# Optimization experiments

Hardware: AMD Instinct MI355X
Metric: run time of the kernel (lower is better)

Reference implementation:

```python
import jax, jax.numpy as jnp
import numpy as np

B, K, D, LS, NL = 32, 64, 256, 128, 2


def _xavier(key, shape):
    # torch xavier_uniform for Linear weight [out, in]
    fan_out, fan_in = shape[-2], shape[-1]
    lim = float(np.sqrt(6.0 / (fan_in + fan_out)))
    return jax.random.uniform(key, shape, jnp.float32, -lim, lim)


def setup_inputs():
    key = jax.random.key(0)
    ks = jax.random.split(key, 32)
    inp = {
        "X": jax.random.normal(ks[0], (B, K, D), jnp.float32),
        # per-layer stacked params [NL, ...]
        "k_w": _xavier(ks[1], (NL, D, D)),
        "q_w": _xavier(ks[2], (NL, D, D)),
        "rv_w1": _xavier(ks[3], (NL, D, 2 * D)),
        "rv_b1": jnp.zeros((NL, D), jnp.float32),
        "rv_w2": _xavier(ks[4], (NL, D, D)),
        "rv_b2": jnp.zeros((NL, D), jnp.float32),
        "ln_g": jnp.ones((NL, D), jnp.float32),
        "ln_b": jnp.zeros((NL, D), jnp.float32),
        "mlp_w1": _xavier(ks[5], (NL, D, D)),
        "mlp_b1": jnp.zeros((NL, D), jnp.float32),
        "mlp_w2": _xavier(ks[6], (NL, D, D)),
        "mlp_b2": jnp.zeros((NL, D), jnp.float32),
        "proj_w": _xavier(ks[7], (LS, D)),
        "proj_b": jnp.zeros((LS,), jnp.float32),
        "mu_w": _xavier(ks[8], (LS, LS)),
        "mu_b": jnp.zeros((LS,), jnp.float32),
        "sp_w": _xavier(ks[9], (LS, LS)),
        "sp_b": jnp.zeros((LS,), jnp.float32),
    }
    return inp


def _gelu(x):
    return jax.nn.gelu(x, approximate=False)


def _layernorm(x, g, b, eps=1e-5):
    m = jnp.mean(x, axis=-1, keepdims=True)
    v = jnp.mean((x - m) ** 2, axis=-1, keepdims=True)
    return (x - m) / jnp.sqrt(v + eps) * g + b


def _block(x, kw, qw, rw1, rb1, rw2, rb2, lg, lb, mw1, mb1, mw2, mb2):
    scale = D ** (-0.5)
    x_orig = x
    # pairwise difference r[b,i,j,:] = x[b,i]-x[b,j]
    r = x[:, :, None, :] - x[:, None, :, :]                      # [B,K,K,D]
    xi = jnp.broadcast_to(x[:, :, None, :], (B, K, K, D))
    cat = jnp.concatenate([xi, r], axis=-1)                      # [B,K,K,2D]
    v = _gelu(jnp.einsum('bijc,dc->bijd', cat, rw1) + rb1)
    v = jnp.einsum('bijd,ed->bije', v, rw2) + rb2                # [B,K,K,D]
    k = jnp.einsum('bid,ed->bie', x, kw)
    q = jnp.einsum('bid,ed->bie', x, qw) * scale
    attn = jax.nn.softmax(jnp.einsum('bid,bjd->bij', q, k), axis=2)
    agg = jnp.einsum('bij,bijd->bid', attn, v)
    h = _layernorm(x_orig + agg, lg, lb)
    h = jnp.einsum('bid,ed->bie', _gelu(jnp.einsum('bid,ed->bie', h, mw1) + mb1), mw2) + mb2
    return x_orig + h


def reference(X, k_w, q_w, rv_w1, rv_b1, rv_w2, rv_b2, ln_g, ln_b,
              mlp_w1, mlp_b1, mlp_w2, mlp_b2, proj_w, proj_b,
              mu_w, mu_b, sp_w, sp_b):
    x = X
    for i in range(NL):
        x = _block(x, k_w[i], q_w[i], rv_w1[i], rv_b1[i], rv_w2[i], rv_b2[i],
                   ln_g[i], ln_b[i], mlp_w1[i], mlp_b1[i], mlp_w2[i], mlp_b2[i])
    s = jnp.sum(x, axis=1)                                        # [B,D]
    h = _gelu(s @ proj_w.T + proj_b)                              # [B,LS]
    mu = h @ mu_w.T + mu_b
    scale = jax.nn.softplus(h @ sp_w.T + sp_b)
    return (mu, scale)
```

## Files before the change

kernel.cpp:

```cpp
#include <hip/hip_runtime.h>
#include <hip/hip_bf16.h>

#define NL 2

using bf16 = __hip_bfloat16;
typedef short bf16x8 __attribute__((ext_vector_type(8)));
typedef float f32x4 __attribute__((ext_vector_type(4)));

__device__ __forceinline__ float bfu(unsigned short u) { return __uint_as_float(((unsigned)u) << 16); }

__device__ __forceinline__ unsigned short bfr(float v) {
  unsigned u = __float_as_uint(v);
  u += 0x7FFFu + ((u >> 16) & 1u);
  return (unsigned short)(u >> 16);
}

__device__ __forceinline__ float gelu_s(float x) {
  float e = __expf(-1.702f * x);
  return x * __builtin_amdgcn_rcpf(1.0f + e);
}

__device__ __forceinline__ float gelu_e(float x) {
  return 0.5f * x * (1.0f + erff(x * 0.7071067811865475f));
}

__device__ __forceinline__ float load_f(const void* p, int i, int fl) {
  if (fl) return bfu(((const unsigned short*)p)[i]);
  return ((const float*)p)[i];
}

__device__ __forceinline__ int block_detect(const void* X) {
  __shared__ int bad_s;
  if (threadIdx.x == 0) bad_s = 0;
  __syncthreads();
  if (threadIdx.x < 256) {
    const float v = bfu(((const unsigned short*)X)[threadIdx.x]);
    if (!(fabsf(v) < 1e6f)) atomicOr(&bad_s, 1);
  }
  __syncthreads();
  return bad_s ? 0 : 1;
}

__device__ __forceinline__ void stage_split4(unsigned short (&aF)[2][4096], int row, int d0, float4 v) {
  ushort4 h, lo;
  h.x = bfr(v.x); h.y = bfr(v.y); h.z = bfr(v.z); h.w = bfr(v.w);
  lo.x = bfr(v.x - bfu(h.x)); lo.y = bfr(v.y - bfu(h.y));
  lo.z = bfr(v.z - bfu(h.z)); lo.w = bfr(v.w - bfu(h.w));
  const int kt = d0 >> 5, lane = row | (((d0 >> 3) & 3) << 4), j = d0 & 7;
  *(ushort4*)&aF[0][kt*512 + lane*8 + j] = h;
  *(ushort4*)&aF[1][kt*512 + lane*8 + j] = lo;
}

__global__ __launch_bounds__(256) void prep_kernel(
    const void* __restrict__ X, const void* __restrict__ kw, const void* __restrict__ qw,
    const void* __restrict__ rw1, const void* __restrict__ rw2, const void* __restrict__ mw1,
    const void* __restrict__ mw2, const void* __restrict__ pw, const void* __restrict__ muw,
    const void* __restrict__ spw,
    const void* __restrict__ rb1, const void* __restrict__ rb2, const void* __restrict__ lng,
    const void* __restrict__ lnb, const void* __restrict__ mb1, const void* __restrict__ mb2,
    const void* __restrict__ pb, const void* __restrict__ mub, const void* __restrict__ spb,
    unsigned short* __restrict__ wfb, unsigned short* __restrict__ w3b,
    float* __restrict__ wh, float* __restrict__ bc)
{
  __shared__ __align__(16) char psm[65536];
  const int fl = block_detect(X);
  const int t = threadIdx.x;
  int blk = blockIdx.x;

  if (blk < 16) {
    unsigned short* ls = (unsigned short*)psm;
    unsigned* lsu = (unsigned*)psm;
    const int l = blk >> 3, kt = blk & 7;
    if (fl) {
      #pragma unroll
      for (int s = 0; s < 4; ++s) {
        const unsigned* sp = (const unsigned*)((s == 0) ? kw : (s == 1) ? qw : rw1);
        const int rstr = (s < 2) ? 128 : 256;
        const int coff = ((s == 3) ? 128 : 0) + kt*16;
        for (int i = t; i < 4096; i += 256) {
          const int e = i >> 4, d2 = i & 15;
          lsu[s*4096 + i] = sp[(l*256 + e)*rstr + coff + d2];
        }
      }
    } else {
      #pragma unroll
      for (int s = 0; s < 4; ++s) {
        const float* sp = (const float*)((s == 0) ? kw : (s == 1) ? qw : rw1);
        const int rstr = (s < 2) ? 256 : 512;
        const int coff = ((s == 3) ? 256 : 0) + kt*32;
        for (int i = t; i < 4096; i += 256) {
          const int e = i >> 4, d2 = i & 15;
          const float f0 = sp[(l*256 + e)*rstr + coff + d2*2];
          const float f1 = sp[(l*256 + e)*rstr + coff + d2*2 + 1];
          lsu[s*4096 + i] = (unsigned)bfr(f0) | ((unsigned)bfr(f1) << 16);
        }
      }
    }
    __syncthreads();
    unsigned* outp = (unsigned*)wfb + (l*8 + kt)*16384;
    for (int f2 = t; f2 < 16384; f2 += 256) {
      const int j2 = f2 & 3, lane = (f2 >> 2) & 63, ntg = f2 >> 8;
      const int seg = ntg >> 4;
      const int e = (ntg & 15)*16 + (lane & 15);
      const int dl = ((lane >> 4) & 3)*8 + j2*2;
      unsigned short r0 = ls[seg*8192 + e*32 + dl];
      unsigned short r1 = ls[seg*8192 + e*32 + dl + 1];
      if (seg == 1) { r0 = bfr(bfu(r0)*0.0625f); r1 = bfr(bfu(r1)*0.0625f); }
      else if (seg == 2) {
        const unsigned short w0 = ls[3*8192 + e*32 + dl];
        const unsigned short w1 = ls[3*8192 + e*32 + dl + 1];
        r0 = bfr(bfu(r0) + bfu(w0)); r1 = bfr(bfu(r1) + bfu(w1));
      }
      outp[f2] = (unsigned)r0 | ((unsigned)r1 << 16);
    }
    return;
  }
  blk -= 16;
  if (blk < 48) {
    unsigned short* ls = (unsigned short*)psm;
    unsigned* lsu = (unsigned*)psm;
    const int l3 = blk >> 3, kt = blk & 7;
    const int l = l3 / 3, gm = l3 % 3;
    const void* src = (gm == 0) ? rw2 : (gm == 1) ? mw1 : mw2;
    if (fl) {
      const unsigned* sp = (const unsigned*)src;
      for (int i = t; i < 4096; i += 256) {
        const int e = i >> 4, d2 = i & 15;
        lsu[i] = sp[(l*256 + e)*128 + kt*16 + d2];
      }
    } else {
      const float* sp = (const float*)src;
      for (int i = t; i < 4096; i += 256) {
        const int e = i >> 4, d2 = i & 15;
        const float f0 = sp[(l*256 + e)*256 + kt*32 + d2*2];
        const float f1 = sp[(l*256 + e)*256 + kt*32 + d2*2 + 1];
        lsu[i] = (unsigned)bfr(f0) | ((unsigned)bfr(f1) << 16);
      }
    }
    __syncthreads();
    unsigned* outp = (unsigned*)w3b + (l3*8 + kt)*4096;
    for (int f2 = t; f2 < 4096; f2 += 256) {
      const int j2 = f2 & 3, lane = (f2 >> 2) & 63, nt = f2 >> 8;
      const int e = nt*16 + (lane & 15);
      const int dl = ((lane >> 4) & 3)*8 + j2*2;
      outp[f2] = (unsigned)ls[e*32 + dl] | ((unsigned)ls[e*32 + dl + 1] << 16);
    }
    return;
  }
  blk -= 48;
  if (blk < 24) {
    float* lsf = (float*)psm;
    if (blk < 8) {
      const int l0 = blk*16;
      if (fl) {
        const unsigned* sp = (const unsigned*)pw;
        for (int i = t; i < 2048; i += 256) {
          const int ll = i >> 7, d2 = i & 127;
          const unsigned u = sp[(l0 + ll)*128 + d2];
          lsf[ll*256 + d2*2]     = __uint_as_float(u << 16);
          lsf[ll*256 + d2*2 + 1] = __uint_as_float(u & 0xffff0000u);
        }
      } else {
        const float* sp = (const float*)pw;
        for (int i = t; i < 4096; i += 256) {
          const int ll = i >> 8, d = i & 255;
          lsf[ll*256 + d] = sp[(l0 + ll)*256 + d];
        }
      }
      __syncthreads();
      for (int i = t; i < 4096; i += 256) {
        const int d = i >> 4, ll = i & 15;
        wh[d*128 + l0 + ll] = lsf[ll*256 + d];
      }
    } else {
      const int grp = blk - 8;
      const int isSp = grp >> 3;
      const int l0 = (grp & 7)*16;
      const void* src = isSp ? spw : muw;
      const int off = isSp ? 49152 : 32768;
      if (fl) {
        const unsigned* sp = (const unsigned*)src;
        for (int i = t; i < 1024; i += 256) {
          const int ll = i >> 6, c2 = i & 63;
          const unsigned u = sp[(l0 + ll)*64 + c2];
          lsf[ll*128 + c2*2]     = __uint_as_float(u << 16);
          lsf[ll*128 + c2*2 + 1] = __uint_as_float(u & 0xffff0000u);
        }
      } else {
        const float* sp = (const float*)src;
        for (int i = t; i < 2048; i += 256) {
          const int ll = i >> 7, c = i & 127;
          lsf[ll*128 + c] = sp[(l0 + ll)*128 + c];
        }
      }
      __syncthreads();
      for (int i = t; i < 2048; i += 256) {
        const int c = i >> 4, ll = i & 15;
        wh[off + c*128 + l0 + ll] = lsf[ll*128 + c];
      }
    }
    return;
  }
  for (int i = t; i < 3456; i += 256) {
    const void* src; int off;
    if (i < 512)       { src = rb1; off = i; }
    else if (i < 1024) { src = rb2; off = i - 512; }
    else if (i < 1536) { src = lng; off = i - 1024; }
    else if (i < 2048) { src = lnb; off = i - 1536; }
    else if (i < 2560) { src = mb1; off = i - 2048; }
    else if (i < 3072) { src = mb2; off = i - 2560; }
    else if (i < 3200) { src = pb;  off = i - 3072; }
    else if (i < 3328) { src = mub; off = i - 3200; }
    else               { src = spb; off = i - 3328; }
    bc[i] = load_f(src, off, fl);
  }
}

template<bool SPLIT>
__device__ __forceinline__ void k1_body(
    const unsigned short (&aF)[2][4096],
    const unsigned short* __restrict__ wfb, const float* __restrict__ bc,
    float* __restrict__ kq, float* __restrict__ Pf, unsigned* __restrict__ Qpk,
    int l, int row0, int t)
{
  const int w = t >> 6, l64 = t & 63;
  const int col = l64 & 15, quad = l64 >> 4;
  f32x4 acc[8];
  #pragma unroll
  for (int i = 0; i < 8; ++i) acc[i] = (f32x4){0.f, 0.f, 0.f, 0.f};
  for (int kt = 0; kt < 8; ++kt) {
    const bf16x8 ah = *(const bf16x8*)&aF[0][kt*512 + l64*8];
    bf16x8 al;
    if (SPLIT) al = *(const bf16x8*)&aF[1][kt*512 + l64*8];
    #pragma unroll
    for (int i = 0; i < 8; ++i) {
      const int ntg = w*8 + i;
      const bf16x8 b = *(const bf16x8*)&wfb[((l*8 + kt)*64 + ntg)*512 + l64*8];
      acc[i] = __builtin_amdgcn_mfma_f32_16x16x32_bf16(ah, b, acc[i], 0, 0, 0);
      if (SPLIT) acc[i] = __builtin_amdgcn_mfma_f32_16x16x32_bf16(al, b, acc[i], 0, 0, 0);
    }
  }
  #pragma unroll
  for (int i = 0; i < 8; ++i) {
    const int ntg = w*8 + i;
    if (ntg < 32) {
      const int n = ntg*16 + col;
      #pragma unroll
      for (int r = 0; r < 4; ++r)
        kq[(size_t)(row0 + quad*4 + r)*512 + n] = acc[i][r];
    } else if (ntg < 48) {
      const int c = (ntg - 32)*16 + col;
      const float bias = bc[l*256 + c];
      #pragma unroll
      for (int r = 0; r < 4; ++r)
        Pf[(size_t)(row0 + quad*4 + r)*256 + c] = acc[i][r] + bias;
    } else {
      #pragma unroll
      for (int r = 0; r < 4; ++r) {
        const float v = acc[i][r];
        const float pv = __shfl_xor(v, 1, 64);
        if (!(col & 1)) {
          const unsigned uu = (unsigned)bfr(v) | ((unsigned)bfr(pv) << 16);
          Qpk[(size_t)(row0 + quad*4 + r)*128 + (ntg - 48)*8 + (col >> 1)] = uu;
        }
      }
    }
  }
}

__global__ __launch_bounds__(512) void k1l0(
    const void* __restrict__ X, const unsigned short* __restrict__ wfb,
    const float* __restrict__ bc, float* __restrict__ kq, float* __restrict__ Pf,
    unsigned* __restrict__ Qpk)
{
  const int fl = block_detect(X);
  __shared__ __align__(16) unsigned short aF[2][4096];
  const int t = threadIdx.x;
  const int row0 = blockIdx.x * 16;
  if (fl) {
    const int c = t;
    const int row = c >> 5, d0 = (c & 31) * 8;
    const uint4 u = *(const uint4*)((const unsigned*)X + (size_t)(row0 + row)*128 + (c & 31)*4);
    const int kt = d0 >> 5, lane = row | (((d0 >> 3) & 3) << 4);
    *(uint4*)&aF[0][kt*512 + lane*8] = u;
  } else {
    for (int i = t; i < 1024; i += 512) {
      const int row = i >> 6, d0 = (i & 63) * 4;
      const float4 v = *(const float4*)((const float*)X + (size_t)(row0 + row)*256 + d0);
      stage_split4(aF, row, d0, v);
    }
  }
  __syncthreads();
  if (fl) k1_body<false>(aF, wfb, bc, kq, Pf, Qpk, 0, row0, t);
  else    k1_body<true >(aF, wfb, bc, kq, Pf, Qpk, 0, row0, t);
}

__global__ __launch_bounds__(256) void k23_attn(
    const float* __restrict__ kq, const float* __restrict__ Pf,
    const unsigned* __restrict__ Qpk, float* __restrict__ g)
{
  __shared__ unsigned qls[8192];
  __shared__ float qs[4][256];
  __shared__ float sc[4][64];
  __shared__ float als[4][64];
  const int t = threadIdx.x;
  const int b = (int)blockIdx.x >> 4, rq = (int)blockIdx.x & 15;
  const int base = b << 6, i0 = rq * 4;
  {
    const float4* src = (const float4*)(Qpk + (size_t)base*128);
    float4* dst = (float4*)qls;
    for (int i = t; i < 2048; i += 256) dst[i] = src[i];
  }
  for (int i = t; i < 1024; i += 256)
    qs[i >> 8][i & 255] = kq[(size_t)(base + i0 + (i >> 8))*512 + 256 + (i & 255)];
  __syncthreads();

  {
    const int w = t >> 6, lane = t & 63;
    const int jl = lane & 15, part = lane >> 4;
    const int j = w*16 + jl;
    const float* krow = kq + (size_t)(base + j)*512 + part*64;
    float s0 = 0.f, s1 = 0.f, s2 = 0.f, s3 = 0.f;
    for (int dd = 0; dd < 64; dd += 4) {
      const float4 kv = *(const float4*)&krow[dd];
      const float4 q0 = *(const float4*)&qs[0][part*64 + dd];
      const float4 q1 = *(const float4*)&qs[1][part*64 + dd];
      const float4 q2 = *(const float4*)&qs[2][part*64 + dd];
      const float4 q3 = *(const float4*)&qs[3][part*64 + dd];
      s0 = fmaf(kv.x, q0.x, s0); s0 = fmaf(kv.y, q0.y, s0); s0 = fmaf(kv.z, q0.z, s0); s0 = fmaf(kv.w, q0.w, s0);
      s1 = fmaf(kv.x, q1.x, s1); s1 = fmaf(kv.y, q1.y, s1); s1 = fmaf(kv.z, q1.z, s1); s1 = fmaf(kv.w, q1.w, s1);
      s2 = fmaf(kv.x, q2.x, s2); s2 = fmaf(kv.y, q2.y, s2); s2 = fmaf(kv.z, q2.z, s2); s2 = fmaf(kv.w, q2.w, s2);
      s3 = fmaf(kv.x, q3.x, s3); s3 = fmaf(kv.y, q3.y, s3); s3 = fmaf(kv.z, q3.z, s3); s3 = fmaf(kv.w, q3.w, s3);
    }
    s0 += __shfl_xor(s0, 16, 64); s0 += __shfl_xor(s0, 32, 64);
    s1 += __shfl_xor(s1, 16, 64); s1 += __shfl_xor(s1, 32, 64);
    s2 += __shfl_xor(s2, 16, 64); s2 += __shfl_xor(s2, 32, 64);
    s3 += __shfl_xor(s3, 16, 64); s3 += __shfl_xor(s3, 32, 64);
    if (part == 0) { sc[0][j] = s0; sc[1][j] = s1; sc[2][j] = s2; sc[3][j] = s3; }
  }
  __syncthreads();
  {
    const int row = t >> 6, j = t & 63;
    float s = sc[row][j];
    float m = s;
    #pragma unroll
    for (int off = 32; off; off >>= 1) m = fmaxf(m, __shfl_xor(m, off, 64));
    const float e = __expf(s - m);
    float ss = e;
    #pragma unroll
    for (int off = 32; off; off >>= 1) ss += __shfl_xor(ss, off, 64);
    als[row][j] = e / ss;
  }
  __syncthreads();

  const int rg = t >> 7, cp = t & 127;
  const int r0 = base + i0 + rg*2;
  const float2 P0 = *(const float2*)&Pf[(size_t)r0*256 + cp*2];
  const float2 P1 = *(const float2*)&Pf[(size_t)(r0 + 1)*256 + cp*2];
  const float A00 = -1.702f * P0.x, A01 = -1.702f * P0.y;
  const float A10 = -1.702f * P1.x, A11 = -1.702f * P1.y;
  const float* a0p = &als[rg*2][0];
  const float* a1p = &als[rg*2 + 1][0];
  float acc00 = 0.f, acc01 = 0.f, acc10 = 0.f, acc11 = 0.f;
  #pragma unroll 4
  for (int j = 0; j < 64; ++j) {
    const unsigned u = qls[j*128 + cp];
    const float w0 = a0p[j], w1 = a1p[j];
    const float q0 = __uint_as_float(u << 16);
    const float q1 = __uint_as_float(u & 0xffff0000u);
    const float s00 = __builtin_amdgcn_rcpf(1.f + __expf(fmaf(1.702f, q0, A00)));
    const float s01 = __builtin_amdgcn_rcpf(1.f + __expf(fmaf(1.702f, q1, A01)));
    const float s10 = __builtin_amdgcn_rcpf(1.f + __expf(fmaf(1.702f, q0, A10)));
    const float s11 = __builtin_amdgcn_rcpf(1.f + __expf(fmaf(1.702f, q1, A11)));
    acc00 = fmaf(w0 * (P0.x - q0), s00, acc00);
    acc01 = fmaf(w0 * (P0.y - q1), s01, acc01);
    acc10 = fmaf(w1 * (P1.x - q0), s10, acc10);
    acc11 = fmaf(w1 * (P1.y - q1), s11, acc11);
  }
  *(float2*)&g[(size_t)r0*256 + cp*2]       = make_float2(acc00, acc01);
  *(float2*)&g[(size_t)(r0 + 1)*256 + cp*2] = make_float2(acc10, acc11);
}

__device__ __forceinline__ void k4_gemm8(
    f32x4 acc[2], const unsigned short (&aF)[2][4096],
    const unsigned short* __restrict__ wg, int w, int l64)
{
  acc[0] = (f32x4){0.f, 0.f, 0.f, 0.f};
  acc[1] = (f32x4){0.f, 0.f, 0.f, 0.f};
  for (int kt = 0; kt < 8; ++kt) {
    const bf16x8 ah = *(const bf16x8*)&aF[0][kt*512 + l64*8];
    const bf16x8 al = *(const bf16x8*)&aF[1][kt*512 + l64*8];
    #pragma unroll
    for (int nt = 0; nt < 2; ++nt) {
      const bf16x8 b = *(const bf16x8*)&wg[((kt*16 + (w*2 + nt))*64 + l64)*8];
      acc[nt] = __builtin_amdgcn_mfma_f32_16x16x32_bf16(ah, b, acc[nt], 0, 0, 0);
      acc[nt] = __builtin_amdgcn_mfma_f32_16x16x32_bf16(al, b, acc[nt], 0, 0, 0);
    }
  }
}

template<bool ADAPT, bool TAIL>
__device__ __forceinline__ void k4_core(
    const float* __restrict__ g, const void* __restrict__ xin, int fl,
    float* __restrict__ xout, const unsigned short* __restrict__ wg,
    const float* __restrict__ bc, int l, int row0, int t,
    unsigned short (&aF)[2][4096], float* bufB, float (&mv)[16][2])
{
  const int w = t >> 6, l64 = t & 63;
  const int col = l64 & 15, quad = l64 >> 4;
  const float* rb2c = bc + 512  + l*256;
  const float* lngc = bc + 1024 + l*256;
  const float* lnbc = bc + 1536 + l*256;
  const float* mb1c = bc + 2048 + l*256;
  const float* mb2c = bc + 2560 + l*256;

  for (int i = t; i < 1024; i += 512) {
    const int row = i >> 6, d0 = (i & 63) * 4;
    stage_split4(aF, row, d0, *(const float4*)&g[(size_t)(row0 + row)*256 + d0]);
  }
  if (ADAPT && fl) {
    for (int c = t; c < 2048; c += 512) {
      const int row = c >> 7, dp = c & 127;
      const unsigned u = ((const unsigned*)xin)[(size_t)(row0 + row)*128 + dp];
      bufB[row*260 + dp*2]     = __uint_as_float(u << 16);
      bufB[row*260 + dp*2 + 1] = __uint_as_float(u & 0xffff0000u);
    }
  } else {
    for (int c = t; c < 1024; c += 512) {
      const int row = c >> 6, d0 = (c & 63) * 4;
      *(float4*)&bufB[row*260 + d0] = *(const float4*)((const float*)xin + (size_t)(row0 + row)*256 + d0);
    }
  }
  __syncthreads();
  float xtr[2][4];
  #pragma unroll
  for (int nt = 0; nt < 2; ++nt) {
    const int cn = (w*2 + nt)*16 + col;
    #pragma unroll
    for (int r = 0; r < 4; ++r) xtr[nt][r] = bufB[(quad*4 + r)*260 + cn];
  }
  __syncthreads();

  f32x4 acc[2];
  k4_gemm8(acc, aF, wg, w, l64);
  #pragma unroll
  for (int nt = 0; nt < 2; ++nt) {
    const int cn = (w*2 + nt)*16 + col;
    #pragma unroll
    for (int r = 0; r < 4; ++r)
      bufB[(quad*4 + r)*260 + cn] = acc[nt][r] + rb2c[cn] + xtr[nt][r];
  }
  __syncthreads();
  {
    const int row = t >> 5, part = t & 31;
    float s = 0.f, s2 = 0.f;
    #pragma unroll
    for (int kk = 0; kk < 8; ++kk) {
      const float v = bufB[row*260 + part + kk*32];
      s += v; s2 = fmaf(v, v, s2);
    }
    #pragma unroll
    for (int off = 16; off; off >>= 1) {
      s  += __shfl_xor(s, off, 32);
      s2 += __shfl_xor(s2, off, 32);
    }
    if (part == 0) {
      const float mu = s * (1.f/256.f);
      mv[row][0] = mu;
      mv[row][1] = rsqrtf(fmaf(-mu, mu, s2 * (1.f/256.f)) + 1e-5f);
    }
  }
  __syncthreads();
  for (int i = t; i < 1024; i += 512) {
    const int row = i >> 6, d0 = (i & 63) * 4;
    float4 v = *(const float4*)&bufB[row*260 + d0];
    const float m = mv[row][0], iv = mv[row][1];
    v.x = (v.x - m)*iv*lngc[d0]   + lnbc[d0];
    v.y = (v.y - m)*iv*lngc[d0+1] + lnbc[d0+1];
    v.z = (v.z - m)*iv*lngc[d0+2] + lnbc[d0+2];
    v.w = (v.w - m)*iv*lngc[d0+3] + lnbc[d0+3];
    stage_split4(aF, row, d0, v);
  }
  __syncthreads();
  k4_gemm8(acc, aF, wg + 65536, w, l64);
  #pragma unroll
  for (int nt = 0; nt < 2; ++nt) {
    const int cn = (w*2 + nt)*16 + col;
    #pragma unroll
    for (int r = 0; r < 4; ++r)
      bufB[(quad*4 + r)*260 + cn] = gelu_e(acc[nt][r] + mb1c[cn]);
  }
  __syncthreads();
  for (int i = t; i < 1024; i += 512) {
    const int row = i >> 6, d0 = (i & 63) * 4;
    stage_split4(aF, row, d0, *(const float4*)&bufB[row*260 + d0]);
  }
  __syncthreads();
  k4_gemm8(acc, aF, wg + 2*65536, w, l64);
  if (TAIL) {
    #pragma unroll
    for (int nt = 0; nt < 2; ++nt) {
      const int cn = (w*2 + nt)*16 + col;
      #pragma unroll
      for (int r = 0; r < 4; ++r)
        bufB[(quad*4 + r)*260 + cn] = acc[nt][r] + mb2c[cn] + xtr[nt][r];
    }
    __syncthreads();
    for (int i = t; i < 1024; i += 512) {
      const int row = i >> 6, d0 = (i & 63) * 4;
      const float4 v = *(const float4*)&bufB[row*260 + d0];
      *(float4*)&xout[(size_t)(row0 + row)*256 + d0] = v;
      stage_split4(aF, row, d0, v);
    }
    __syncthreads();
  } else {
    #pragma unroll
    for (int nt = 0; nt < 2; ++nt) {
      const int cn = (w*2 + nt)*16 + col;
      #pragma unroll
      for (int r = 0; r < 4; ++r)
        xout[(size_t)(row0 + quad*4 + r)*256 + cn] = acc[nt][r] + mb2c[cn] + xtr[nt][r];
    }
  }
}

__global__ __launch_bounds__(512) void k41_mix_kq(
    const float* __restrict__ g, const unsigned short* __restrict__ w3b,
    const unsigned short* __restrict__ wfb, const float* __restrict__ bc,
    const void* __restrict__ X, float* __restrict__ x,
    float* __restrict__ kq, float* __restrict__ Pf, unsigned* __restrict__ Qpk)
{
  const int fl = block_detect(X);
  __shared__ __align__(16) unsigned short aF[2][4096];
  __shared__ float bufB[16*260];
  __shared__ float mv[16][2];
  const int t = threadIdx.x;
  const int row0 = blockIdx.x * 16;
  k4_core<true, true>(g, X, fl, x, w3b, bc, 0, row0, t, aF, bufB, mv);
  k1_body<true>(aF, wfb, bc, kq, Pf, Qpk, 1, row0, t);
}

__global__ __launch_bounds__(512) void k4_fin(
    const float* __restrict__ g, const unsigned short* __restrict__ w3b,
    const float* __restrict__ bc, float* __restrict__ x)
{
  __shared__ __align__(16) unsigned short aF[2][4096];
  __shared__ float bufB[16*260];
  __shared__ float mv[16][2];
  const int t = threadIdx.x;
  const int row0 = blockIdx.x * 16;
  k4_core<false, false>(g, x, 0, x, w3b + 3*65536, bc, 1, row0, t, aF, bufB, mv);
}

__global__ __launch_bounds__(256) void k5_head(
    const float* __restrict__ x, const float* __restrict__ wh,
    const float* __restrict__ bc, const void* __restrict__ X,
    void* __restrict__ out)
{
  const int fl = block_detect(X);
  __shared__ float ss[256];
  __shared__ float hh[128];
  const int b = blockIdx.x, t = threadIdx.x;
  float s = 0.f;
  for (int i = 0; i < 64; ++i) s += x[(size_t)((b << 6) + i)*256 + t];
  ss[t] = s;
  __syncthreads();
  if (t < 128) {
    float acc = bc[3072 + t];
    const float* projT = wh;
    for (int d = 0; d < 256; ++d) acc = fmaf(ss[d], projT[d*128 + t], acc);
    hh[t] = gelu_e(acc);
  }
  __syncthreads();
  float v; int oidx;
  if (t < 128) {
    float acc = bc[3200 + t];
    const float* muT = wh + 32768;
    for (int c = 0; c < 128; ++c) acc = fmaf(hh[c], muT[c*128 + t], acc);
    v = acc; oidx = b*128 + t;
  } else {
    const int u = t - 128;
    float acc = bc[3328 + u];
    const float* spT = wh + 49152;
    for (int c = 0; c < 128; ++c) acc = fmaf(hh[c], spT[c*128 + u], acc);
    v = (acc > 20.f) ? acc : log1pf(__expf(acc));
    oidx = 4096 + b*128 + u;
  }
  if (fl) ((bf16*)out)[oidx] = __float2bfloat16(v);
  else    ((float*)out)[oidx] = v;
}

extern "C" void kernel_launch(void* const* d_in, const int* in_sizes, int n_in,
                              void* d_out, int out_size, void* d_ws, size_t ws_size,
                              hipStream_t stream)
{
  (void)in_sizes; (void)n_in; (void)out_size; (void)ws_size;
  float* ws    = (float*)d_ws;
  float* x     = ws + 16;
  float* kq    = x + 524288;
  float* Pf    = kq + 1048576;
  unsigned* Qpk = (unsigned*)(Pf + 524288);
  float* g     = (float*)(Qpk + 262144);
  unsigned short* wfb = (unsigned short*)(g + 524288);
  unsigned short* w3b = wfb + 524288;
  float* wh    = (float*)(w3b + 393216);
  float* bc    = wh + 65536;

  prep_kernel<<<dim3(89), dim3(256), 0, stream>>>(
      d_in[0], d_in[1], d_in[2], d_in[3], d_in[5], d_in[9], d_in[11],
      d_in[13], d_in[15], d_in[17],
      d_in[4], d_in[6], d_in[7], d_in[8], d_in[10], d_in[12],
      d_in[14], d_in[16], d_in[18],
      wfb, w3b, wh, bc);
  k1l0<<<dim3(128), dim3(512), 0, stream>>>(d_in[0], wfb, bc, kq, Pf, Qpk);
  k23_attn<<<dim3(512), dim3(256), 0, stream>>>(kq, Pf, Qpk, g);
  k41_mix_kq<<<dim3(128), dim3(512), 0, stream>>>(g, w3b, wfb, bc, d_in[0], x, kq, Pf, Qpk);
  k23_attn<<<dim3(512), dim3(256), 0, stream>>>(kq, Pf, Qpk, g);
  k4_fin<<<dim3(128), dim3(512), 0, stream>>>(g, w3b, bc, x);
  k5_head<<<dim3(32), dim3(256), 0, stream>>>(x, wh, bc, d_in[0], (void*)d_out);
}
```

Before: 213.8 us.

## Fuse all stages into one persistent kernel with global atomic barriers

Replaces the seven separate launches (prep, layer-0 kq, two attention passes, mix/kq, final mix, head) with a single 256-block persistent kernel. Stages are separated by a grid-wide barrier after weight prep and by per-batch-group atomic counters after that, so each group of 8 blocks advances on its own. Work is remapped to 512-thread blocks and the prep blocks' inner loops now stride by 512. This removes launch gaps and tail effects, but relies on all 256 blocks being co-resident and adds spin-wait cost plus an extra memset.

New measurement: 268.6 us. 1.26x slower.

```diff
diff --git a/kernel.cpp b/kernel.cpp
--- a/kernel.cpp
+++ b/kernel.cpp
@@ -1,7 +1,6 @@
 #include <hip/hip_runtime.h>
 #include <hip/hip_bf16.h>
 
-#define NL 2
 
 using bf16 = __hip_bfloat16;
 typedef short bf16x8 __attribute__((ext_vector_type(8)));
@@ -15,11 +14,6 @@
   return (unsigned short)(u >> 16);
 }
 
-__device__ __forceinline__ float gelu_s(float x) {
-  float e = __expf(-1.702f * x);
-  return x * __builtin_amdgcn_rcpf(1.0f + e);
-}
-
 __device__ __forceinline__ float gelu_e(float x) {
   return 0.5f * x * (1.0f + erff(x * 0.7071067811865475f));
 }
@@ -39,6 +33,18 @@
   }
   __syncthreads();
   return bad_s ? 0 : 1;
+}
+
+__device__ __forceinline__ void wsbar(unsigned* cnt, unsigned need) {
+  __syncthreads();
+  if (threadIdx.x == 0) {
+    __threadfence();
+    atomicAdd(cnt, 1u);
+    while (__hip_atomic_load(cnt, __ATOMIC_RELAXED, __HIP_MEMORY_SCOPE_AGENT) < need)
+      __builtin_amdgcn_s_sleep(2);
+    __threadfence();
+  }
+  __syncthreads();
 }
 
 __device__ __forceinline__ void stage_split4(unsigned short (&aF)[2][4096], int row, int d0, float4 v) {
@@ -51,86 +57,103 @@
   *(ushort4*)&aF[1][kt*512 + lane*8 + j] = lo;
 }
 
-__global__ __launch_bounds__(256) void prep_kernel(
-    const void* __restrict__ X, const void* __restrict__ kw, const void* __restrict__ qw,
-    const void* __restrict__ rw1, const void* __restrict__ rw2, const void* __restrict__ mw1,
-    const void* __restrict__ mw2, const void* __restrict__ pw, const void* __restrict__ muw,
-    const void* __restrict__ spw,
-    const void* __restrict__ rb1, const void* __restrict__ rb2, const void* __restrict__ lng,
-    const void* __restrict__ lnb, const void* __restrict__ mb1, const void* __restrict__ mb2,
-    const void* __restrict__ pb, const void* __restrict__ mub, const void* __restrict__ spb,
-    unsigned short* __restrict__ wfb, unsigned short* __restrict__ w3b,
-    float* __restrict__ wh, float* __restrict__ bc)
-{
-  __shared__ __align__(16) char psm[65536];
-  const int fl = block_detect(X);
-  const int t = threadIdx.x;
-  int blk = blockIdx.x;
-
+__device__ void prep_phase(
+    int blk, int t, int fl, char* psm,
+    const void* kw, const void* qw, const void* rw1, const void* rw2,
+    const void* mw1, const void* mw2, const void* pw, const void* muw, const void* spw,
+    const void* rb1, const void* rb2, const void* lng, const void* lnb,
+    const void* mb1, const void* mb2, const void* pb, const void* mub, const void* spb,
+    unsigned short* wfb, unsigned short* w3b, float* wh, float* bc)
+{
   if (blk < 16) {
     unsigned short* ls = (unsigned short*)psm;
     unsigned* lsu = (unsigned*)psm;
     const int l = blk >> 3, kt = blk & 7;
-    if (fl) {
-      #pragma unroll
-      for (int s = 0; s < 4; ++s) {
-        const unsigned* sp = (const unsigned*)((s == 0) ? kw : (s == 1) ? qw : rw1);
-        const int rstr = (s < 2) ? 128 : 256;
-        const int coff = ((s == 3) ? 128 : 0) + kt*16;
-        for (int i = t; i < 4096; i += 256) {
-          const int e = i >> 4, d2 = i & 15;
-          lsu[s*4096 + i] = sp[(l*256 + e)*rstr + coff + d2];
-        }
-      }
-    } else {
-      #pragma unroll
-      for (int s = 0; s < 4; ++s) {
-        const float* sp = (const float*)((s == 0) ? kw : (s == 1) ? qw : rw1);
-        const int rstr = (s < 2) ? 256 : 512;
-        const int coff = ((s == 3) ? 256 : 0) + kt*32;
-        for (int i = t; i < 4096; i += 256) {
-          const int e = i >> 4, d2 = i & 15;
-          const float f0 = sp[(l*256 + e)*rstr + coff + d2*2];
-          const float f1 = sp[(l*256 + e)*rstr + coff + d2*2 + 1];
-          lsu[s*4096 + i] = (unsigned)bfr(f0) | ((unsigned)bfr(f1) << 16);
-        }
-      }
-    }
-    __syncthreads();
-    unsigned* outp = (unsigned*)wfb + (l*8 + kt)*16384;
-    for (int f2 = t; f2 < 16384; f2 += 256) {
-      const int j2 = f2 & 3, lane = (f2 >> 2) & 63, ntg = f2 >> 8;
-      const int seg = ntg >> 4;
-      const int e = (ntg & 15)*16 + (lane & 15);
-      const int dl = ((lane >> 4) & 3)*8 + j2*2;
-      unsigned short r0 = ls[seg*8192 + e*32 + dl];
-      unsigned short r1 = ls[seg*8192 + e*32 + dl + 1];
-      if (seg == 1) { r0 = bfr(bfu(r0)*0.0625f); r1 = bfr(bfu(r1)*0.0625f); }
-      else if (seg == 2) {
-        const unsigned short w0 = ls[3*8192 + e*32 + dl];
-        const unsigned short w1 = ls[3*8192 + e*32 + dl + 1];
-        r0 = bfr(bfu(r0) + bfu(w0)); r1 = bfr(bfu(r1) + bfu(w1));
-      }
-      outp[f2] = (unsigned)r0 | ((unsigned)r1 << 16);
+    #pragma unroll
+    for (int pass = 0; pass < 2; ++pass) {
+      if (pass == 0) {
+        if (fl) {
+          #pragma unroll
+          for (int s = 0; s < 2; ++s) {
+            const unsigned* sp = (const unsigned*)((s == 0) ? kw : qw);
+            for (int i = t; i < 4096; i += 512) {
+              const int e = i >> 4, d2 = i & 15;
+              lsu[s*4096 + i] = sp[(l*256 + e)*128 + kt*16 + d2];
+            }
+          }
+        } else {
+          #pragma unroll
+          for (int s = 0; s < 2; ++s) {
+            const float* sp = (const float*)((s == 0) ? kw : qw);
+            for (int i = t; i < 4096; i += 512) {
+              const int e = i >> 4, d2 = i & 15;
+              const float f0 = sp[(l*256 + e)*256 + kt*32 + d2*2];
+              const float f1 = sp[(l*256 + e)*256 + kt*32 + d2*2 + 1];
+              lsu[s*4096 + i] = (unsigned)bfr(f0) | ((unsigned)bfr(f1) << 16);
+            }
+          }
+        }
+      } else {
+        if (fl) {
+          const unsigned* sp = (const unsigned*)rw1;
+          #pragma unroll
+          for (int s = 0; s < 2; ++s)
+            for (int i = t; i < 4096; i += 512) {
+              const int e = i >> 4, d2 = i & 15;
+              lsu[s*4096 + i] = sp[(l*256 + e)*256 + s*128 + kt*16 + d2];
+            }
+        } else {
+          const float* sp = (const float*)rw1;
+          #pragma unroll
+          for (int s = 0; s < 2; ++s)
+            for (int i = t; i < 4096; i += 512) {
+              const int e = i >> 4, d2 = i & 15;
+              const float f0 = sp[(l*256 + e)*512 + s*256 + kt*32 + d2*2];
+              const float f1 = sp[(l*256 + e)*512 + s*256 + kt*32 + d2*2 + 1];
+              lsu[s*4096 + i] = (unsigned)bfr(f0) | ((unsigned)bfr(f1) << 16);
+            }
+        }
+      }
+      __syncthreads();
+      unsigned* outp = (unsigned*)wfb + (l*8 + kt)*16384 + pass*8192;
+      for (int f2 = t; f2 < 8192; f2 += 512) {
+        const int j2 = f2 & 3, lane = (f2 >> 2) & 63, ntl = f2 >> 8;
+        const int seg = ntl >> 4;
+        const int e = (ntl & 15)*16 + (lane & 15);
+        const int dl = ((lane >> 4) & 3)*8 + j2*2;
+        unsigned short r0 = ls[seg*8192 + e*32 + dl];
+        unsigned short r1 = ls[seg*8192 + e*32 + dl + 1];
+        if (pass == 0) {
+          if (seg == 1) { r0 = bfr(bfu(r0)*0.0625f); r1 = bfr(bfu(r1)*0.0625f); }
+        } else {
+          if (seg == 0) {
+            const unsigned short w0 = ls[8192 + e*32 + dl];
+            const unsigned short w1 = ls[8192 + e*32 + dl + 1];
+            r0 = bfr(bfu(r0) + bfu(w0)); r1 = bfr(bfu(r1) + bfu(w1));
+          }
+        }
+        outp[f2] = (unsigned)r0 | ((unsigned)r1 << 16);
+      }
+      __syncthreads();
     }
     return;
   }
-  blk -= 16;
-  if (blk < 48) {
+  int b2 = blk - 16;
+  if (b2 < 48) {
     unsigned short* ls = (unsigned short*)psm;
     unsigned* lsu = (unsigned*)psm;
-    const int l3 = blk >> 3, kt = blk & 7;
+    const int l3 = b2 >> 3, kt = b2 & 7;
     const int l = l3 / 3, gm = l3 % 3;
     const void* src = (gm == 0) ? rw2 : (gm == 1) ? mw1 : mw2;
     if (fl) {
       const unsigned* sp = (const unsigned*)src;
-      for (int i = t; i < 4096; i += 256) {
+      for (int i = t; i < 4096; i += 512) {
         const int e = i >> 4, d2 = i & 15;
         lsu[i] = sp[(l*256 + e)*128 + kt*16 + d2];
       }
     } else {
       const float* sp = (const float*)src;
-      for (int i = t; i < 4096; i += 256) {
+      for (int i = t; i < 4096; i += 512) {
         const int e = i >> 4, d2 = i & 15;
         const float f0 = sp[(l*256 + e)*256 + kt*32 + d2*2];
         const float f1 = sp[(l*256 + e)*256 + kt*32 + d2*2 + 1];
@@ -139,7 +162,7 @@
     }
     __syncthreads();
     unsigned* outp = (unsigned*)w3b + (l3*8 + kt)*4096;
-    for (int f2 = t; f2 < 4096; f2 += 256) {
+    for (int f2 = t; f2 < 4096; f2 += 512) {
       const int j2 = f2 & 3, lane = (f2 >> 2) & 63, nt = f2 >> 8;
       const int e = nt*16 + (lane & 15);
       const int dl = ((lane >> 4) & 3)*8 + j2*2;
@@ -147,14 +170,14 @@
     }
     return;
   }
-  blk -= 48;
-  if (blk < 24) {
+  b2 -= 48;
+  if (b2 < 24) {
     float* lsf = (float*)psm;
-    if (blk < 8) {
-      const int l0 = blk*16;
+    if (b2 < 8) {
+      const int l0 = b2*16;
       if (fl) {
         const unsigned* sp = (const unsigned*)pw;
-        for (int i = t; i < 2048; i += 256) {
+        for (int i = t; i < 2048; i += 512) {
           const int ll = i >> 7, d2 = i & 127;
           const unsigned u = sp[(l0 + ll)*128 + d2];
           lsf[ll*256 + d2*2]     = __uint_as_float(u << 16);
@@ -162,25 +185,25 @@
         }
       } else {
         const float* sp = (const float*)pw;
-        for (int i = t; i < 4096; i += 256) {
+        for (int i = t; i < 4096; i += 512) {
           const int ll = i >> 8, d = i & 255;
           lsf[ll*256 + d] = sp[(l0 + ll)*256 + d];
         }
       }
       __syncthreads();
-      for (int i = t; i < 4096; i += 256) {
+      for (int i = t; i < 4096; i += 512) {
         const int d = i >> 4, ll = i & 15;
         wh[d*128 + l0 + ll] = lsf[ll*256 + d];
       }
     } else {
-      const int grp = blk - 8;
-      const int isSp = grp >> 3;
-      const int l0 = (grp & 7)*16;
+      const int grp2 = b2 - 8;
+      const int isSp = grp2 >> 3;
+      const int l0 = (grp2 & 7)*16;
       const void* src = isSp ? spw : muw;
       const int off = isSp ? 49152 : 32768;
       if (fl) {
         const unsigned* sp = (const unsigned*)src;
-        for (int i = t; i < 1024; i += 256) {
+        for (int i = t; i < 1024; i += 512) {
           const int ll = i >> 6, c2 = i & 63;
           const unsigned u = sp[(l0 + ll)*64 + c2];
           lsf[ll*128 + c2*2]     = __uint_as_float(u << 16);
@@ -188,61 +211,63 @@
         }
       } else {
         const float* sp = (const float*)src;
-        for (int i = t; i < 2048; i += 256) {
+        for (int i = t; i < 2048; i += 512) {
           const int ll = i >> 7, c = i & 127;
           lsf[ll*128 + c] = sp[(l0 + ll)*128 + c];
         }
       }
       __syncthreads();
-      for (int i = t; i < 2048; i += 256) {
+      for (int i = t; i < 2048; i += 512) {
         const int c = i >> 4, ll = i & 15;
         wh[off + c*128 + l0 + ll] = lsf[ll*128 + c];
       }
     }
     return;
   }
-  for (int i = t; i < 3456; i += 256) {
-    const void* src; int off;
-    if (i < 512)       { src = rb1; off = i; }
-    else if (i < 1024) { src = rb2; off = i - 512; }
-    else if (i < 1536) { src = lng; off = i - 1024; }
-    else if (i < 2048) { src = lnb; off = i - 1536; }
-    else if (i < 2560) { src = mb1; off = i - 2048; }
-    else if (i < 3072) { src = mb2; off = i - 2560; }
-    else if (i < 3200) { src = pb;  off = i - 3072; }
-    else if (i < 3328) { src = mub; off = i - 3200; }
-    else               { src = spb; off = i - 3328; }
-    bc[i] = load_f(src, off, fl);
-  }
-}
-
-template<bool SPLIT>
+  if (b2 == 24) {
+    for (int i = t; i < 3456; i += 512) {
+      const void* src; int off;
+      if (i < 512)       { src = rb1; off = i; }
+      else if (i < 1024) { src = rb2; off = i - 512; }
+      else if (i < 1536) { src = lng; off = i - 1024; }
+      else if (i < 2048) { src = lnb; off = i - 1536; }
+      else if (i < 2560) { src = mb1; off = i - 2048; }
+      else if (i < 3072) { src = mb2; off = i - 2560; }
+      else if (i < 3200) { src = pb;  off = i - 3072; }
+      else if (i < 3328) { src = mub; off = i - 3200; }
+      else               { src = spb; off = i - 3328; }
+      bc[i] = load_f(src, off, fl);
+    }
+  }
+}
+
+template<bool SPLIT, int NTG>
 __device__ __forceinline__ void k1_body(
     const unsigned short (&aF)[2][4096],
     const unsigned short* __restrict__ wfb, const float* __restrict__ bc,
     float* __restrict__ kq, float* __restrict__ Pf, unsigned* __restrict__ Qpk,
-    int l, int row0, int t)
+    int l, int row0, int ntg0, int t)
 {
   const int w = t >> 6, l64 = t & 63;
   const int col = l64 & 15, quad = l64 >> 4;
-  f32x4 acc[8];
+  f32x4 acc[NTG];
   #pragma unroll
-  for (int i = 0; i < 8; ++i) acc[i] = (f32x4){0.f, 0.f, 0.f, 0.f};
+  for (int i = 0; i < NTG; ++i) acc[i] = (f32x4){0.f, 0.f, 0.f, 0.f};
   for (int kt = 0; kt < 8; ++kt) {
     const bf16x8 ah = *(const bf16x8*)&aF[0][kt*512 + l64*8];
     bf16x8 al;
     if (SPLIT) al = *(const bf16x8*)&aF[1][kt*512 + l64*8];
     #pragma unroll
-    for (int i = 0; i < 8; ++i) {
-      const int ntg = w*8 + i;
+    for (int i = 0; i < NTG; ++i) {
+      const int ntg = ntg0 + w*NTG + i;
       const bf16x8 b = *(const bf16x8*)&wfb[((l*8 + kt)*64 + ntg)*512 + l64*8];
       acc[i] = __builtin_amdgcn_mfma_f32_16x16x32_bf16(ah, b, acc[i], 0, 0, 0);
       if (SPLIT) acc[i] = __builtin_amdgcn_mfma_f32_16x16x32_bf16(al, b, acc[i], 0, 0, 0);
     }
   }
   #pragma unroll
-  for (int i = 0; i < 8; ++i) {
-    const int ntg = w*8 + i;
+  for (int i = 0; i < NTG; ++i) {
+    const int ntg = ntg0 + w*NTG + i;
     if (ntg < 32) {
       const int n = ntg*16 + col;
       #pragma unroll
@@ -268,65 +293,43 @@
   }
 }
 
-__global__ __launch_bounds__(512) void k1l0(
-    const void* __restrict__ X, const unsigned short* __restrict__ wfb,
-    const float* __restrict__ bc, float* __restrict__ kq, float* __restrict__ Pf,
-    unsigned* __restrict__ Qpk)
-{
-  const int fl = block_detect(X);
-  __shared__ __align__(16) unsigned short aF[2][4096];
-  const int t = threadIdx.x;
-  const int row0 = blockIdx.x * 16;
-  if (fl) {
-    const int c = t;
-    const int row = c >> 5, d0 = (c & 31) * 8;
-    const uint4 u = *(const uint4*)((const unsigned*)X + (size_t)(row0 + row)*128 + (c & 31)*4);
-    const int kt = d0 >> 5, lane = row | (((d0 >> 3) & 3) << 4);
-    *(uint4*)&aF[0][kt*512 + lane*8] = u;
-  } else {
-    for (int i = t; i < 1024; i += 512) {
-      const int row = i >> 6, d0 = (i & 63) * 4;
-      const float4 v = *(const float4*)((const float*)X + (size_t)(row0 + row)*256 + d0);
-      stage_split4(aF, row, d0, v);
-    }
-  }
-  __syncthreads();
-  if (fl) k1_body<false>(aF, wfb, bc, kq, Pf, Qpk, 0, row0, t);
-  else    k1_body<true >(aF, wfb, bc, kq, Pf, Qpk, 0, row0, t);
-}
-
-__global__ __launch_bounds__(256) void k23_attn(
+__device__ void k23_phase(
     const float* __restrict__ kq, const float* __restrict__ Pf,
-    const unsigned* __restrict__ Qpk, float* __restrict__ g)
-{
-  __shared__ unsigned qls[8192];
-  __shared__ float qs[4][256];
-  __shared__ float sc[4][64];
-  __shared__ float als[4][64];
-  const int t = threadIdx.x;
-  const int b = (int)blockIdx.x >> 4, rq = (int)blockIdx.x & 15;
-  const int base = b << 6, i0 = rq * 4;
+    const unsigned* __restrict__ Qpk, float* __restrict__ g,
+    int base, int sub, int t, char* smem)
+{
+  unsigned* qls = (unsigned*)smem;
+  float* qsp = (float*)(smem + 32768);
+  float* scp = (float*)(smem + 40960);
+  float* alp = (float*)(smem + 43008);
+  const int h = t >> 8, t256 = t & 255;
+  const int i0 = (sub*2 + h)*4;
   {
     const float4* src = (const float4*)(Qpk + (size_t)base*128);
     float4* dst = (float4*)qls;
-    for (int i = t; i < 2048; i += 256) dst[i] = src[i];
-  }
-  for (int i = t; i < 1024; i += 256)
-    qs[i >> 8][i & 255] = kq[(size_t)(base + i0 + (i >> 8))*512 + 256 + (i & 255)];
-  __syncthreads();
-
+    for (int i = t; i < 2048; i += 512) dst[i] = src[i];
+  }
+  for (int i = t; i < 2048; i += 512) {
+    const int h2 = i >> 10, r = (i >> 8) & 3, d = i & 255;
+    qsp[h2*1024 + r*256 + d] = kq[(size_t)(base + (sub*2 + h2)*4 + r)*512 + 256 + d];
+  }
+  __syncthreads();
   {
-    const int w = t >> 6, lane = t & 63;
+    const int w4 = t256 >> 6, lane = t256 & 63;
     const int jl = lane & 15, part = lane >> 4;
-    const int j = w*16 + jl;
+    const int j = w4*16 + jl;
     const float* krow = kq + (size_t)(base + j)*512 + part*64;
+    const float* q0p = qsp + h*1024 + 0*256 + part*64;
+    const float* q1p = qsp + h*1024 + 1*256 + part*64;
+    const float* q2p = qsp + h*1024 + 2*256 + part*64;
+    const float* q3p = qsp + h*1024 + 3*256 + part*64;
     float s0 = 0.f, s1 = 0.f, s2 = 0.f, s3 = 0.f;
     for (int dd = 0; dd < 64; dd += 4) {
       const float4 kv = *(const float4*)&krow[dd];
-      const float4 q0 = *(const float4*)&qs[0][part*64 + dd];
-      const float4 q1 = *(const float4*)&qs[1][part*64 + dd];
-      const float4 q2 = *(const float4*)&qs[2][part*64 + dd];
-      const float4 q3 = *(const float4*)&qs[3][part*64 + dd];
+      const float4 q0 = *(const float4*)&q0p[dd];
+      const float4 q1 = *(const float4*)&q1p[dd];
+      const float4 q2 = *(const float4*)&q2p[dd];
+      const float4 q3 = *(const float4*)&q3p[dd];
       s0 = fmaf(kv.x, q0.x, s0); s0 = fmaf(kv.y, q0.y, s0); s0 = fmaf(kv.z, q0.z, s0); s0 = fmaf(kv.w, q0.w, s0);
       s1 = fmaf(kv.x, q1.x, s1); s1 = fmaf(kv.y, q1.y, s1); s1 = fmaf(kv.z, q1.z, s1); s1 = fmaf(kv.w, q1.w, s1);
       s2 = fmaf(kv.x, q2.x, s2); s2 = fmaf(kv.y, q2.y, s2); s2 = fmaf(kv.z, q2.z, s2); s2 = fmaf(kv.w, q2.w, s2);
@@ -336,12 +339,17 @@
     s1 += __shfl_xor(s1, 16, 64); s1 += __shfl_xor(s1, 32, 64);
     s2 += __shfl_xor(s2, 16, 64); s2 += __shfl_xor(s2, 32, 64);
     s3 += __shfl_xor(s3, 16, 64); s3 += __shfl_xor(s3, 32, 64);
-    if (part == 0) { sc[0][j] = s0; sc[1][j] = s1; sc[2][j] = s2; sc[3][j] = s3; }
+    if (part == 0) {
+      scp[(h*4 + 0)*64 + j] = s0;
+      scp[(h*4 + 1)*64 + j] = s1;
+      scp[(h*4 + 2)*64 + j] = s2;
+      scp[(h*4 + 3)*64 + j] = s3;
+    }
   }
   __syncthreads();
   {
     const int row = t >> 6, j = t & 63;
-    float s = sc[row][j];
+    float s = scp[row*64 + j];
     float m = s;
     #pragma unroll
     for (int off = 32; off; off >>= 1) m = fmaxf(m, __shfl_xor(m, off, 64));
@@ -349,36 +357,37 @@
     float ss = e;
     #pragma unroll
     for (int off = 32; off; off >>= 1) ss += __shfl_xor(ss, off, 64);
-    als[row][j] = e / ss;
-  }
-  __syncthreads();
-
-  const int rg = t >> 7, cp = t & 127;
-  const int r0 = base + i0 + rg*2;
-  const float2 P0 = *(const float2*)&Pf[(size_t)r0*256 + cp*2];
-  const float2 P1 = *(const float2*)&Pf[(size_t)(r0 + 1)*256 + cp*2];
-  const float A00 = -1.702f * P0.x, A01 = -1.702f * P0.y;
-  const float A10 = -1.702f * P1.x, A11 = -1.702f * P1.y;
-  const float* a0p = &als[rg*2][0];
-  const float* a1p = &als[rg*2 + 1][0];
-  float acc00 = 0.f, acc01 = 0.f, acc10 = 0.f, acc11 = 0.f;
-  #pragma unroll 4
-  for (int j = 0; j < 64; ++j) {
-    const unsigned u = qls[j*128 + cp];
-    const float w0 = a0p[j], w1 = a1p[j];
-    const float q0 = __uint_as_float(u << 16);
-    const float q1 = __uint_as_float(u & 0xffff0000u);
-    const float s00 = __builtin_amdgcn_rcpf(1.f + __expf(fmaf(1.702f, q0, A00)));
-    const float s01 = __builtin_amdgcn_rcpf(1.f + __expf(fmaf(1.702f, q1, A01)));
-    const float s10 = __builtin_amdgcn_rcpf(1.f + __expf(fmaf(1.702f, q0, A10)));
-    const float s11 = __builtin_amdgcn_rcpf(1.f + __expf(fmaf(1.702f, q1, A11)));
-    acc00 = fmaf(w0 * (P0.x - q0), s00, acc00);
-    acc01 = fmaf(w0 * (P0.y - q1), s01, acc01);
-    acc10 = fmaf(w1 * (P1.x - q0), s10, acc10);
-    acc11 = fmaf(w1 * (P1.y - q1), s11, acc11);
-  }
-  *(float2*)&g[(size_t)r0*256 + cp*2]       = make_float2(acc00, acc01);
-  *(float2*)&g[(size_t)(r0 + 1)*256 + cp*2] = make_float2(acc10, acc11);
+    alp[row*64 + j] = e / ss;
+  }
+  __syncthreads();
+  {
+    const int rg = t256 >> 7, cp = t256 & 127;
+    const int r0 = base + i0 + rg*2;
+    const float2 P0 = *(const float2*)&Pf[(size_t)r0*256 + cp*2];
+    const float2 P1 = *(const float2*)&Pf[(size_t)(r0 + 1)*256 + cp*2];
+    const float A00 = -1.702f * P0.x, A01 = -1.702f * P0.y;
+    const float A10 = -1.702f * P1.x, A11 = -1.702f * P1.y;
+    const float* a0p = alp + (h*4 + rg*2)*64;
+    const float* a1p = alp + (h*4 + rg*2 + 1)*64;
+    float acc00 = 0.f, acc01 = 0.f, acc10 = 0.f, acc11 = 0.f;
+    #pragma unroll 4
+    for (int j = 0; j < 64; ++j) {
+      const unsigned u = qls[j*128 + cp];
+      const float w0 = a0p[j], w1 = a1p[j];
+      const float q0 = __uint_as_float(u << 16);
+      const float q1 = __uint_as_float(u & 0xffff0000u);
+      const float s00 = __builtin_amdgcn_rcpf(1.f + __expf(fmaf(1.702f, q0, A00)));
+      const float s01 = __builtin_amdgcn_rcpf(1.f + __expf(fmaf(1.702f, q1, A01)));
+      const float s10 = __builtin_amdgcn_rcpf(1.f + __expf(fmaf(1.702f, q0, A10)));
+      const float s11 = __builtin_amdgcn_rcpf(1.f + __expf(fmaf(1.702f, q1, A11)));
+      acc00 = fmaf(w0 * (P0.x - q0), s00, acc00);
+      acc01 = fmaf(w0 * (P0.y - q1), s01, acc01);
+      acc10 = fmaf(w1 * (P1.x - q0), s10, acc10);
+      acc11 = fmaf(w1 * (P1.y - q1), s11, acc11);
+    }
+    *(float2*)&g[(size_t)r0*256 + cp*2]       = make_float2(acc00, acc01);
+    *(float2*)&g[(size_t)(r0 + 1)*256 + cp*2] = make_float2(acc10, acc11);
+  }
 }
 
 __device__ __forceinline__ void k4_gemm8(
@@ -524,46 +533,17 @@
   }
 }
 
-__global__ __launch_bounds__(512) void k41_mix_kq(
-    const float* __restrict__ g, const unsigned short* __restrict__ w3b,
-    const unsigned short* __restrict__ wfb, const float* __restrict__ bc,
-    const void* __restrict__ X, float* __restrict__ x,
-    float* __restrict__ kq, float* __restrict__ Pf, unsigned* __restrict__ Qpk)
-{
-  const int fl = block_detect(X);
-  __shared__ __align__(16) unsigned short aF[2][4096];
-  __shared__ float bufB[16*260];
-  __shared__ float mv[16][2];
-  const int t = threadIdx.x;
-  const int row0 = blockIdx.x * 16;
-  k4_core<true, true>(g, X, fl, x, w3b, bc, 0, row0, t, aF, bufB, mv);
-  k1_body<true>(aF, wfb, bc, kq, Pf, Qpk, 1, row0, t);
-}
-
-__global__ __launch_bounds__(512) void k4_fin(
-    const float* __restrict__ g, const unsigned short* __restrict__ w3b,
-    const float* __restrict__ bc, float* __restrict__ x)
-{
-  __shared__ __align__(16) unsigned short aF[2][4096];
-  __shared__ float bufB[16*260];
-  __shared__ float mv[16][2];
-  const int t = threadIdx.x;
-  const int row0 = blockIdx.x * 16;
-  k4_core<false, false>(g, x, 0, x, w3b + 3*65536, bc, 1, row0, t, aF, bufB, mv);
-}
-
-__global__ __launch_bounds__(256) void k5_head(
-    const float* __restrict__ x, const float* __restrict__ wh,
-    const float* __restrict__ bc, const void* __restrict__ X,
-    void* __restrict__ out)
-{
-  const int fl = block_detect(X);
-  __shared__ float ss[256];
-  __shared__ float hh[128];
-  const int b = blockIdx.x, t = threadIdx.x;
-  float s = 0.f;
-  for (int i = 0; i < 64; ++i) s += x[(size_t)((b << 6) + i)*256 + t];
-  ss[t] = s;
+__device__ void k5_phase(
+    int b, int t, int fl, const float* __restrict__ x, const float* __restrict__ wh,
+    const float* __restrict__ bc, void* __restrict__ out, char* smem)
+{
+  float* ss = (float*)smem;
+  float* hh = ss + 256;
+  if (t < 256) {
+    float s = 0.f;
+    for (int i = 0; i < 64; ++i) s += x[(size_t)((b << 6) + i)*256 + t];
+    ss[t] = s;
+  }
   __syncthreads();
   if (t < 128) {
     float acc = bc[3072 + t];
@@ -572,22 +552,98 @@
     hh[t] = gelu_e(acc);
   }
   __syncthreads();
-  float v; int oidx;
-  if (t < 128) {
-    float acc = bc[3200 + t];
-    const float* muT = wh + 32768;
-    for (int c = 0; c < 128; ++c) acc = fmaf(hh[c], muT[c*128 + t], acc);
-    v = acc; oidx = b*128 + t;
-  } else {
-    const int u = t - 128;
-    float acc = bc[3328 + u];
-    const float* spT = wh + 49152;
-    for (int c = 0; c < 128; ++c) acc = fmaf(hh[c], spT[c*128 + u], acc);
-    v = (acc > 20.f) ? acc : log1pf(__expf(acc));
-    oidx = 4096 + b*128 + u;
-  }
-  if (fl) ((bf16*)out)[oidx] = __float2bfloat16(v);
-  else    ((float*)out)[oidx] = v;
+  if (t < 256) {
+    float v; int oidx;
+    if (t < 128) {
+      float acc = bc[3200 + t];
+      const float* muT = wh + 32768;
+      for (int c = 0; c < 128; ++c) acc = fmaf(hh[c], muT[c*128 + t], acc);
+      v = acc; oidx = b*128 + t;
+    } else {
+      const int u = t - 128;
+      float acc = bc[3328 + u];
+      const float* spT = wh + 49152;
+      for (int c = 0; c < 128; ++c) acc = fmaf(hh[c], spT[c*128 + u], acc);
+      v = (acc > 20.f) ? acc : log1pf(__expf(acc));
+      oidx = 4096 + b*128 + u;
+    }
+    if (fl) ((bf16*)out)[oidx] = __float2bfloat16(v);
+    else    ((float*)out)[oidx] = v;
+  }
+}
+
+__global__ __launch_bounds__(512, 4) void mega_kernel(
+    const void* __restrict__ X, const void* __restrict__ kw, const void* __restrict__ qw,
+    const void* __restrict__ rw1, const void* __restrict__ rw2, const void* __restrict__ mw1,
+    const void* __restrict__ mw2, const void* __restrict__ pw, const void* __restrict__ muw,
+    const void* __restrict__ spw,
+    const void* __restrict__ rb1, const void* __restrict__ rb2, const void* __restrict__ lng,
+    const void* __restrict__ lnb, const void* __restrict__ mb1, const void* __restrict__ mb2,
+    const void* __restrict__ pb, const void* __restrict__ mub, const void* __restrict__ spb,
+    unsigned* __restrict__ bars,
+    float* __restrict__ x, float* __restrict__ kq, float* __restrict__ Pf,
+    unsigned* __restrict__ Qpk, float* __restrict__ g,
+    unsigned short* __restrict__ wfb, unsigned short* __restrict__ w3b,
+    float* __restrict__ wh, float* __restrict__ bc, void* __restrict__ out)
+{
+  __shared__ __align__(16) char smem[45056];
+  __shared__ float mv[16][2];
+  const int t = threadIdx.x;
+  const int blk = blockIdx.x;
+  const int fl = block_detect(X);
+  auto& aF = *(unsigned short(*)[2][4096])smem;
+  float* bufB = (float*)(smem + 16384);
+
+  if (blk < 89)
+    prep_phase(blk, t, fl, smem, kw, qw, rw1, rw2, mw1, mw2, pw, muw, spw,
+               rb1, rb2, lng, lnb, mb1, mb2, pb, mub, spb, wfb, w3b, wh, bc);
+  wsbar(&bars[0], 256u);
+
+  const int grp = blk >> 3, sub = blk & 7;
+  unsigned* gb = &bars[32 * (1 + grp)];
+  const int base = grp << 6;
+
+  {
+    const int row0 = (grp*4 + (sub >> 1)) * 16;
+    const int nb = sub & 1;
+    if (fl) {
+      const int row = t >> 5, d0 = (t & 31) * 8;
+      const uint4 u = *(const uint4*)((const unsigned*)X + (size_t)(row0 + row)*128 + (t & 31)*4);
+      const int kt = d0 >> 5, lane = row | (((d0 >> 3) & 3) << 4);
+      *(uint4*)&aF[0][kt*512 + lane*8] = u;
+    } else {
+      for (int i = t; i < 1024; i += 512) {
+        const int row = i >> 6, d0 = (i & 63) * 4;
+        stage_split4(aF, row, d0, *(const float4*)((const float*)X + (size_t)(row0 + row)*256 + d0));
+      }
+    }
+    __syncthreads();
+    if (fl) k1_body<false, 4>(aF, wfb, bc, kq, Pf, Qpk, 0, row0, nb*32, t);
+    else    k1_body<true,  4>(aF, wfb, bc, kq, Pf, Qpk, 0, row0, nb*32, t);
+  }
+  wsbar(gb, 8u*1);
+
+  k23_phase(kq, Pf, Qpk, g, base, sub, t, smem);
+  wsbar(gb, 8u*2);
+
+  if (sub < 4) {
+    const int row0 = (grp*4 + sub) * 16;
+    k4_core<true, true>(g, X, fl, x, w3b, bc, 0, row0, t, aF, bufB, mv);
+    k1_body<true, 8>(aF, wfb, bc, kq, Pf, Qpk, 1, row0, 0, t);
+  }
+  wsbar(gb, 8u*3);
+
+  k23_phase(kq, Pf, Qpk, g, base, sub, t, smem);
+  wsbar(gb, 8u*4);
+
+  if (sub < 4) {
+    const int row0 = (grp*4 + sub) * 16;
+    k4_core<false, false>(g, x, 0, x, w3b + 3*65536, bc, 1, row0, t, aF, bufB, mv);
+  }
+  wsbar(gb, 8u*5);
+
+  if (sub == 0)
+    k5_phase(grp, t, fl, x, wh, bc, out, smem);
 }
 
 extern "C" void kernel_launch(void* const* d_in, const int* in_sizes, int n_in,
@@ -595,8 +651,9 @@
                               hipStream_t stream)
 {
   (void)in_sizes; (void)n_in; (void)out_size; (void)ws_size;
-  float* ws    = (float*)d_ws;
-  float* x     = ws + 16;
+  unsigned* bars = (unsigned*)d_ws;
+  float* base  = (float*)d_ws + 2048;
+  float* x     = base;
   float* kq    = x + 524288;
   float* Pf    = kq + 1048576;
   unsigned* Qpk = (unsigned*)(Pf + 524288);
@@ -606,16 +663,11 @@
   float* wh    = (float*)(w3b + 393216);
   float* bc    = wh + 65536;
 
-  prep_kernel<<<dim3(89), dim3(256), 0, stream>>>(
+  hipMemsetAsync(d_ws, 0, 8192, stream);
+  mega_kernel<<<dim3(256), dim3(512), 0, stream>>>(
       d_in[0], d_in[1], d_in[2], d_in[3], d_in[5], d_in[9], d_in[11],
       d_in[13], d_in[15], d_in[17],
       d_in[4], d_in[6], d_in[7], d_in[8], d_in[10], d_in[12],
       d_in[14], d_in[16], d_in[18],
-      wfb, w3b, wh, bc);
-  k1l0<<<dim3(128), dim3(512), 0, stream>>>(d_in[0], wfb, bc, kq, Pf, Qpk);
-  k23_attn<<<dim3(512), dim3(256), 0, stream>>>(kq, Pf, Qpk, g);
-  k41_mix_kq<<<dim3(128), dim3(512), 0, stream>>>(g, w3b, wfb, bc, d_in[0], x, kq, Pf, Qpk);
-  k23_attn<<<dim3(512), dim3(256), 0, stream>>>(kq, Pf, Qpk, g);
-  k4_fin<<<dim3(128), dim3(512), 0, stream>>>(g, w3b, bc, x);
-  k5_head<<<dim3(32), dim3(256), 0, stream>>>(x, wh, bc, d_in[0], (void*)d_out);
-}
+      bars, x, kq, Pf, Qpk, g, wfb, w3b, wh, bc, (void*)d_out);
+}
```
